# Optimization experiments

Measured on AMD Instinct MI355X. Metric: run time of the kernel, lower is better.

The kernel has to match this reference:

```python
import jax, jax.numpy as jnp
import numpy as np

N_HEADS = 12
MAX_POS = 2048
SEQ = MAX_POS - 2  # seq_len_without_special = 2046
HEAD_DIM = 64
BATCH = 8


def setup_inputs() -> dict:
    key = jax.random.key(0)
    k1, k2, k3 = jax.random.split(key, 3)
    v = jax.random.normal(k1, (BATCH, MAX_POS, N_HEADS, HEAD_DIM), jnp.float32)
    offset = jax.random.normal(k2, (1, N_HEADS), jnp.float32)
    # learned bias base, torch init: uniform(-0.1, 0.1), shape [1, H, SEQ] (symmetric)
    w = jax.random.uniform(k3, (1, N_HEADS, SEQ), jnp.float32, -0.1, 0.1)
    return {"v": v, "offset": offset, "w": w}


def _fft_bias(v, offset, w):
    # strip special tokens ([CLS]/[SEP])
    v_ = v[:, 1:-1, :, :]                      # [B, S, H, D]
    B, S, H, D = v_.shape
    # --- symmetric circulant base z of length 2S-1 ---
    w_ = w[..., :S]                            # [1, H, S]
    z = jnp.concatenate(
        [w_[..., -1:], jnp.flip(w_[..., 1:], axis=-1), w_[..., :-1]], axis=-1
    )                                          # [1, H, 2S-1]
    z = z - offset[..., None]                  # broadcast offset per head
    z = jnp.exp(z)                             # feature_map == 'exp'
    z_fft = jnp.fft.rfft(z)                    # [1, H, S] complex (len 2S-1 odd -> m=S)

    pad = S - 1                                # symmetric: pad_size = seq_len - 1
    v_p = jnp.transpose(v_, (0, 3, 2, 1))      # [B, D, H, S]
    v_p = jnp.pad(v_p, ((0, 0), (0, 0), (0, 0), (pad, 0)))  # left-pad to 2S-1
    v_fft = jnp.fft.rfft(v_p)                  # [B, D, H, S]
    # torch.irfft(x, 1) with default signal_sizes infers even length 2*(m-1)=2S-2
    pbv = jnp.fft.irfft(v_fft * z_fft)[..., :S]  # [B, D, H, S]
    pbv = jnp.pad(pbv, ((0, 0), (0, 0), (0, 0), (1, 1)))     # restore special slots
    pbv = jnp.transpose(pbv, (0, 3, 2, 1))     # [B, S+2, H, D]

    o = jnp.pad(jnp.ones((S,), v.dtype), (pad, 0))           # [2S-1]
    o_fft = jnp.fft.rfft(o)                    # [S]
    z_pb = jnp.fft.irfft(z_fft * o_fft)[..., :S]             # [1, H, S]
    z_pb = jnp.pad(z_pb, ((0, 0), (0, 0), (1, 1)))           # [1, H, S+2]
    z_pb = jnp.swapaxes(z_pb, -2, -1)          # [1, S+2, H]
    return pbv, z_pb


def reference(v, offset, w):
    return _fft_bias(v, offset, w)
```

## Files before the change

kernel.cpp:

```cpp
#include <hip/hip_runtime.h>
#include <hip/hip_bf16.h>

#define BATCH 8
#define MAXPOS 2048
#define SEQ 2046
#define NH 12
#define HD 64
#define CENTER 2047
#define NCSLOT 254
#define TSTEPS 64
#define PLANE (NH * HD)

typedef __attribute__((ext_vector_type(4))) float floatx4;
typedef __attribute__((ext_vector_type(8))) short shortx8;

#define ATILE_BYTES (NH * NCSLOT * 512 * 2)

__global__ __launch_bounds__(256)
void prep_A(const float* __restrict__ w, const float* __restrict__ off,
            ushort* __restrict__ atile) {
    const int cslot = blockIdx.x;
    const int h     = blockIdx.y;
    const int tid   = threadIdx.x;
    const float offh = off[h];
    const float* wh  = w + h * SEQ;
    const int ci   = cslot - 127;
    const int lane = tid >> 2;
    const int jp   = (tid & 3) * 2;
    const int q    = lane >> 4;
    const int m    = lane & 15;
    const int d0   = 16 * ci + q * 8 - m + jp;
    ushort pk[2];
#pragma unroll
    for (int e = 0; e < 2; ++e) {
        int k = d0 + e; k = (k < 0) ? -k : k;
        float val = (k < SEQ) ? __expf(wh[k] - offh) : 0.f;
        __hip_bfloat16 bv = __float2bfloat16(val);
        pk[e] = *(ushort*)&bv;
    }
    *(ushort2*)(atile + ((size_t)(h * NCSLOT + cslot) * 512 + lane * 8 + jp)) = *(ushort2*)pk;
}

__global__ __launch_bounds__(256)
void prep_V(const float* __restrict__ v, ushort* __restrict__ vbf) {
    __shared__ float Ls[32][64];
    const int tc  = blockIdx.x;
    const int h   = blockIdx.y;
    const int b   = blockIdx.z;
    const int tid = threadIdx.x;
#pragma unroll
    for (int i = 0; i < 2; ++i) {
        int idx = tid + 256 * i;
        int row = idx >> 4;
        int c4  = (idx & 15) * 4;
        int t   = tc * 32 + row;
        float4 val = make_float4(0.f, 0.f, 0.f, 0.f);
        if (t < SEQ) val = *(const float4*)(v + ((size_t)(b * MAXPOS + 1 + t) * NH + h) * HD + c4);
        *(float4*)&Ls[row][c4] = val;
    }
    __syncthreads();
    const int wv   = tid >> 6;
    const int lane = tid & 63;
    const int q    = lane >> 4;
    const int dcol = lane & 15;
    ushort pk[8];
#pragma unroll
    for (int j = 0; j < 8; ++j) {
        __hip_bfloat16 bv = __float2bfloat16(Ls[q * 8 + j][wv * 16 + dcol]);
        pk[j] = *(ushort*)&bv;
    }
    *(uint4*)(vbf + ((size_t)((b * NH + h) * TSTEPS + tc) * 4 + wv) * 512 + lane * 8) = *(uint4*)pk;
}

#define LOADA(dst, tc_)                                                        \
    _Pragma("unroll") for (int s = 0; s < 4; ++s)                              \
        dst[s] = *(const shortx8*)(aP + ((tc_) * 2 - s) * 512);
#define LOADB(dst, tc_)                                                        \
    _Pragma("unroll") for (int dt = 0; dt < 4; ++dt)                           \
        dst[dt] = *(const shortx8*)(bP + ((tc_) * 4 + dt) * 512);

__global__ __launch_bounds__(256, 3)
void gemm_pbv(const ushort* __restrict__ atile, const ushort* __restrict__ vbf,
              float* __restrict__ out) {
    const int bid  = blockIdx.x;
    const int slot = bid >> 3;
    const int g    = (bid & 7) * 6 + (slot % 6);
    const int nt   = slot / 6;
    const int h    = g >> 2;
    const int bpair= g & 3;
    const int tid  = threadIdx.x;
    const int wv   = tid >> 6;
    const int lane = tid & 63;
    const int bb   = bpair * 2 + (wv & 1);
    const int sh   = wv >> 1;
    const int sbase= nt * 8 + sh * 4;

    floatx4 acc[4][4];
#pragma unroll
    for (int s = 0; s < 4; ++s)
#pragma unroll
        for (int dt = 0; dt < 4; ++dt) acc[s][dt] = (floatx4){0.f, 0.f, 0.f, 0.f};

    const ushort* aP = atile + ((size_t)h * NCSLOT + (127 - sbase)) * 512 + lane * 8;
    const ushort* bP = vbf + (size_t)(bb * NH + h) * TSTEPS * 4 * 512 + lane * 8;

    shortx8 a0[4], b0[4], a1[4], b1[4];
    LOADA(a0, 0); LOADB(b0, 0);
    for (int tc = 0; tc < TSTEPS; tc += 2) {
        LOADA(a1, tc + 1); LOADB(b1, tc + 1);
#pragma unroll
        for (int s = 0; s < 4; ++s)
#pragma unroll
            for (int dt = 0; dt < 4; ++dt)
                acc[s][dt] = __builtin_amdgcn_mfma_f32_16x16x32_bf16(a0[s], b0[dt], acc[s][dt], 0, 0, 0);
        if (tc + 2 < TSTEPS) { LOADA(a0, tc + 2); LOADB(b0, tc + 2); }
#pragma unroll
        for (int s = 0; s < 4; ++s)
#pragma unroll
            for (int dt = 0; dt < 4; ++dt)
                acc[s][dt] = __builtin_amdgcn_mfma_f32_16x16x32_bf16(a1[s], b1[dt], acc[s][dt], 0, 0, 0);
    }

    const int q    = lane >> 4;
    const int dcol = lane & 15;
    const int n0   = nt * 128 + sh * 64;
#pragma unroll
    for (int s = 0; s < 4; ++s) {
        int nsb = n0 + s * 16 + q * 4;
#pragma unroll
        for (int r = 0; r < 4; ++r) {
            int n = nsb + r;
            if (n < SEQ) {
                float* ob = out + ((size_t)(bb * MAXPOS + 1 + n) * NH + h) * HD + dcol;
#pragma unroll
                for (int dt = 0; dt < 4; ++dt) ob[dt * 16] = acc[s][dt][r];
            }
        }
    }
}

__global__ __launch_bounds__(256)
void zpb_kernel(const float* __restrict__ w, const float* __restrict__ off,
                float* __restrict__ out) {
    __shared__ float Es[SEQ];
    __shared__ float Ss[SEQ];
    __shared__ float wsum[4];
    const int h   = blockIdx.x;
    const int tid = threadIdx.x;
    const int wid = tid >> 6;
    const int lane = tid & 63;
    const float offh = off[h];
    const float* wh  = w + h * SEQ;
    for (int i = tid; i < SEQ; i += 256) Es[i] = __expf(wh[i] - offh);
    __syncthreads();
    const int base = tid * 8;
    float loc[8];
    float s = 0.f;
#pragma unroll
    for (int j = 0; j < 8; ++j) {
        float e = (base + j < SEQ) ? Es[base + j] : 0.f;
        s += e; loc[j] = s;
    }
    float sc = s;
#pragma unroll
    for (int d = 1; d < 64; d <<= 1) {
        float t = __shfl_up(sc, d);
        if (lane >= d) sc += t;
    }
    if (lane == 63) wsum[wid] = sc;
    __syncthreads();
    float woff = 0.f;
    for (int k = 0; k < wid; ++k) woff += wsum[k];
    float prefix = woff + sc - s;
#pragma unroll
    for (int j = 0; j < 8; ++j)
        if (base + j < SEQ) Ss[base + j] = prefix + loc[j];
    __syncthreads();
    const float E0 = Es[0];
    const size_t zb = (size_t)BATCH * MAXPOS * PLANE;
    for (int i = tid; i < SEQ; i += 256)
        out[zb + (size_t)(i + 1) * NH + h] = Ss[i] + Ss[SEQ - 1 - i] - E0;
}

__global__ __launch_bounds__(256)
void zero_bounds_kernel(float* __restrict__ out) {
    const int i = blockIdx.x * 256 + threadIdx.x;
    if (i < 2 * BATCH * PLANE) {
        int side = i / (BATCH * PLANE);
        int r    = i % (BATCH * PLANE);
        int b    = r / PLANE;
        int j    = r % PLANE;
        int p    = side ? (MAXPOS - 1) : 0;
        out[((size_t)b * MAXPOS + p) * PLANE + j] = 0.f;
    }
    if (i < 2 * NH) {
        size_t zb = (size_t)BATCH * MAXPOS * PLANE;
        int p = (i < NH) ? 0 : (MAXPOS - 1);
        out[zb + (size_t)p * NH + (i % NH)] = 0.f;
    }
}

extern "C" void kernel_launch(void* const* d_in, const int* in_sizes, int n_in,
                              void* d_out, int out_size, void* d_ws, size_t ws_size,
                              hipStream_t stream) {
    const float* v   = (const float*)d_in[0];
    const float* off = (const float*)d_in[1];
    const float* w   = (const float*)d_in[2];
    float* out = (float*)d_out;

    ushort* atile = (ushort*)d_ws;
    ushort* vbf   = (ushort*)((char*)d_ws + ATILE_BYTES);

    zero_bounds_kernel<<<48, 256, 0, stream>>>(out);
    zpb_kernel<<<NH, 256, 0, stream>>>(w, off, out);
    prep_A<<<dim3(NCSLOT, NH), 256, 0, stream>>>(w, off, atile);
    prep_V<<<dim3(TSTEPS, NH, BATCH), 256, 0, stream>>>(v, vbf);
    gemm_pbv<<<768, 256, 0, stream>>>(atile, vbf, out);
}
```

Baseline: 155.3 us.

## Fuse small prep kernels and enlarge GEMM per-wave register tile

Merges the zero-bounds, z_pb prefix-sum and A-tile prep kernels into a single launch that dispatches on block index, cutting two kernel launches. The bias GEMM changes from 256-thread blocks with 4x4 tiles per wave to single-wave blocks holding an 8x4 tile for two batches. Each A fragment is now reused across both batches and more rows per load, to reduce global load traffic per MFMA. In exchange, the grid keeps 768 blocks but each is one wave, so the kernel runs far fewer concurrent waves and has much less latency hiding. Accumulator register pressure also rises sharply.

```diff
diff --git a/kernel.cpp b/kernel.cpp
--- a/kernel.cpp
+++ b/kernel.cpp
@@ -6,7 +6,6 @@
 #define SEQ 2046
 #define NH 12
 #define HD 64
-#define CENTER 2047
 #define NCSLOT 254
 #define TSTEPS 64
 #define PLANE (NH * HD)
@@ -17,28 +16,86 @@
 #define ATILE_BYTES (NH * NCSLOT * 512 * 2)
 
 __global__ __launch_bounds__(256)
-void prep_A(const float* __restrict__ w, const float* __restrict__ off,
-            ushort* __restrict__ atile) {
-    const int cslot = blockIdx.x;
-    const int h     = blockIdx.y;
-    const int tid   = threadIdx.x;
-    const float offh = off[h];
-    const float* wh  = w + h * SEQ;
-    const int ci   = cslot - 127;
-    const int lane = tid >> 2;
-    const int jp   = (tid & 3) * 2;
-    const int q    = lane >> 4;
-    const int m    = lane & 15;
-    const int d0   = 16 * ci + q * 8 - m + jp;
-    ushort pk[2];
-#pragma unroll
-    for (int e = 0; e < 2; ++e) {
-        int k = d0 + e; k = (k < 0) ? -k : k;
-        float val = (k < SEQ) ? __expf(wh[k] - offh) : 0.f;
-        __hip_bfloat16 bv = __float2bfloat16(val);
-        pk[e] = *(ushort*)&bv;
-    }
-    *(ushort2*)(atile + ((size_t)(h * NCSLOT + cslot) * 512 + lane * 8 + jp)) = *(ushort2*)pk;
+void small_prep(const float* __restrict__ w, const float* __restrict__ off,
+                ushort* __restrict__ atile, float* __restrict__ out) {
+    __shared__ float Es[SEQ];
+    __shared__ float Ss[SEQ];
+    __shared__ float wsum[4];
+    const int bi  = blockIdx.x;
+    const int tid = threadIdx.x;
+
+    if (bi < NH) {
+        const int h    = bi;
+        const int wid  = tid >> 6;
+        const int lane = tid & 63;
+        const float offh = off[h];
+        const float* wh  = w + h * SEQ;
+        for (int i = tid; i < SEQ; i += 256) Es[i] = __expf(wh[i] - offh);
+        __syncthreads();
+        const int base = tid * 8;
+        float loc[8];
+        float s = 0.f;
+#pragma unroll
+        for (int j = 0; j < 8; ++j) {
+            float e = (base + j < SEQ) ? Es[base + j] : 0.f;
+            s += e; loc[j] = s;
+        }
+        float sc = s;
+#pragma unroll
+        for (int d = 1; d < 64; d <<= 1) {
+            float t = __shfl_up(sc, d);
+            if (lane >= d) sc += t;
+        }
+        if (lane == 63) wsum[wid] = sc;
+        __syncthreads();
+        float woff = 0.f;
+        for (int k = 0; k < wid; ++k) woff += wsum[k];
+        float prefix = woff + sc - s;
+#pragma unroll
+        for (int j = 0; j < 8; ++j)
+            if (base + j < SEQ) Ss[base + j] = prefix + loc[j];
+        __syncthreads();
+        const float E0 = Es[0];
+        const size_t zb = (size_t)BATCH * MAXPOS * PLANE;
+        for (int i = tid; i < SEQ; i += 256)
+            out[zb + (size_t)(i + 1) * NH + h] = Ss[i] + Ss[SEQ - 1 - i] - E0;
+    } else if (bi < NH + NCSLOT * NH) {
+        const int idx   = bi - NH;
+        const int cslot = idx % NCSLOT;
+        const int h     = idx / NCSLOT;
+        const float offh = off[h];
+        const float* wh  = w + h * SEQ;
+        const int ci   = cslot - 127;
+        const int lane = tid >> 2;
+        const int jp   = (tid & 3) * 2;
+        const int q    = lane >> 4;
+        const int m    = lane & 15;
+        const int d0   = 16 * ci + q * 8 - m + jp;
+        ushort pk[2];
+#pragma unroll
+        for (int e = 0; e < 2; ++e) {
+            int k = d0 + e; k = (k < 0) ? -k : k;
+            float val = (k < SEQ) ? __expf(wh[k] - offh) : 0.f;
+            __hip_bfloat16 bv = __float2bfloat16(val);
+            pk[e] = *(ushort*)&bv;
+        }
+        *(ushort2*)(atile + ((size_t)(h * NCSLOT + cslot) * 512 + lane * 8 + jp)) = *(ushort2*)pk;
+    } else {
+        const int i = (bi - NH - NCSLOT * NH) * 256 + tid;
+        if (i < 2 * BATCH * PLANE) {
+            int side = i / (BATCH * PLANE);
+            int r    = i % (BATCH * PLANE);
+            int b    = r / PLANE;
+            int j    = r % PLANE;
+            int p    = side ? (MAXPOS - 1) : 0;
+            out[((size_t)b * MAXPOS + p) * PLANE + j] = 0.f;
+        }
+        if (i < 2 * NH) {
+            size_t zb = (size_t)BATCH * MAXPOS * PLANE;
+            int p = (i < NH) ? 0 : (MAXPOS - 1);
+            out[zb + (size_t)p * NH + (i % NH)] = 0.f;
+        }
+    }
 }
 
 __global__ __launch_bounds__(256)
@@ -72,14 +129,22 @@
     *(uint4*)(vbf + ((size_t)((b * NH + h) * TSTEPS + tc) * 4 + wv) * 512 + lane * 8) = *(uint4*)pk;
 }
 
-#define LOADA(dst, tc_)                                                        \
-    _Pragma("unroll") for (int s = 0; s < 4; ++s)                              \
+#define PREFA(dst, tc_)                                                        \
+    _Pragma("unroll") for (int s = 0; s < 8; ++s)                              \
         dst[s] = *(const shortx8*)(aP + ((tc_) * 2 - s) * 512);
-#define LOADB(dst, tc_)                                                        \
-    _Pragma("unroll") for (int dt = 0; dt < 4; ++dt)                           \
-        dst[dt] = *(const shortx8*)(bP + ((tc_) * 4 + dt) * 512);
-
-__global__ __launch_bounds__(256, 3)
+#define PREFB(dst0, dst1, tc_)                                                 \
+    _Pragma("unroll") for (int dt = 0; dt < 4; ++dt) {                         \
+        dst0[dt] = *(const shortx8*)(bP0 + ((tc_) * 4 + dt) * 512);            \
+        dst1[dt] = *(const shortx8*)(bP1 + ((tc_) * 4 + dt) * 512);            \
+    }
+#define COMPUTE(aa, bb0, bb1)                                                  \
+    _Pragma("unroll") for (int s = 0; s < 8; ++s)                              \
+    _Pragma("unroll") for (int dt = 0; dt < 4; ++dt) {                         \
+        acc[0][s][dt] = __builtin_amdgcn_mfma_f32_16x16x32_bf16(aa[s], bb0[dt], acc[0][s][dt], 0, 0, 0); \
+        acc[1][s][dt] = __builtin_amdgcn_mfma_f32_16x16x32_bf16(aa[s], bb1[dt], acc[1][s][dt], 0, 0, 0); \
+    }
+
+__global__ __launch_bounds__(64, 1)
 void gemm_pbv(const ushort* __restrict__ atile, const ushort* __restrict__ vbf,
               float* __restrict__ out) {
     const int bid  = blockIdx.x;
@@ -87,116 +152,48 @@
     const int g    = (bid & 7) * 6 + (slot % 6);
     const int nt   = slot / 6;
     const int h    = g >> 2;
-    const int bpair= g & 3;
-    const int tid  = threadIdx.x;
-    const int wv   = tid >> 6;
-    const int lane = tid & 63;
-    const int bb   = bpair * 2 + (wv & 1);
-    const int sh   = wv >> 1;
-    const int sbase= nt * 8 + sh * 4;
-
-    floatx4 acc[4][4];
-#pragma unroll
-    for (int s = 0; s < 4; ++s)
-#pragma unroll
-        for (int dt = 0; dt < 4; ++dt) acc[s][dt] = (floatx4){0.f, 0.f, 0.f, 0.f};
-
-    const ushort* aP = atile + ((size_t)h * NCSLOT + (127 - sbase)) * 512 + lane * 8;
-    const ushort* bP = vbf + (size_t)(bb * NH + h) * TSTEPS * 4 * 512 + lane * 8;
-
-    shortx8 a0[4], b0[4], a1[4], b1[4];
-    LOADA(a0, 0); LOADB(b0, 0);
+    const int bp   = g & 3;
+    const int lane = threadIdx.x;
+
+    floatx4 acc[2][8][4];
+#pragma unroll
+    for (int bw = 0; bw < 2; ++bw)
+#pragma unroll
+        for (int s = 0; s < 8; ++s)
+#pragma unroll
+            for (int dt = 0; dt < 4; ++dt) acc[bw][s][dt] = (floatx4){0.f, 0.f, 0.f, 0.f};
+
+    const ushort* aP  = atile + ((size_t)h * NCSLOT + (127 - nt * 8)) * 512 + lane * 8;
+    const ushort* bP0 = vbf + (size_t)(bp * 2 * NH + h) * (TSTEPS * 4 * 512) + lane * 8;
+    const ushort* bP1 = bP0 + (size_t)NH * (TSTEPS * 4 * 512);
+
+    shortx8 a0[8], a1[8], b00[4], b01[4], b10[4], b11[4];
+    PREFA(a0, 0); PREFB(b00, b01, 0);
     for (int tc = 0; tc < TSTEPS; tc += 2) {
-        LOADA(a1, tc + 1); LOADB(b1, tc + 1);
-#pragma unroll
-        for (int s = 0; s < 4; ++s)
-#pragma unroll
-            for (int dt = 0; dt < 4; ++dt)
-                acc[s][dt] = __builtin_amdgcn_mfma_f32_16x16x32_bf16(a0[s], b0[dt], acc[s][dt], 0, 0, 0);
-        if (tc + 2 < TSTEPS) { LOADA(a0, tc + 2); LOADB(b0, tc + 2); }
-#pragma unroll
-        for (int s = 0; s < 4; ++s)
-#pragma unroll
-            for (int dt = 0; dt < 4; ++dt)
-                acc[s][dt] = __builtin_amdgcn_mfma_f32_16x16x32_bf16(a1[s], b1[dt], acc[s][dt], 0, 0, 0);
+        PREFA(a1, tc + 1); PREFB(b10, b11, tc + 1);
+        COMPUTE(a0, b00, b01);
+        if (tc + 2 < TSTEPS) { PREFA(a0, tc + 2); PREFB(b00, b01, tc + 2); }
+        COMPUTE(a1, b10, b11);
     }
 
     const int q    = lane >> 4;
     const int dcol = lane & 15;
-    const int n0   = nt * 128 + sh * 64;
-#pragma unroll
-    for (int s = 0; s < 4; ++s) {
-        int nsb = n0 + s * 16 + q * 4;
-#pragma unroll
-        for (int r = 0; r < 4; ++r) {
-            int n = nsb + r;
-            if (n < SEQ) {
-                float* ob = out + ((size_t)(bb * MAXPOS + 1 + n) * NH + h) * HD + dcol;
-#pragma unroll
-                for (int dt = 0; dt < 4; ++dt) ob[dt * 16] = acc[s][dt][r];
+#pragma unroll
+    for (int bw = 0; bw < 2; ++bw) {
+        const int bb = bp * 2 + bw;
+#pragma unroll
+        for (int s = 0; s < 8; ++s) {
+            int nsb = nt * 128 + s * 16 + q * 4;
+#pragma unroll
+            for (int r = 0; r < 4; ++r) {
+                int n = nsb + r;
+                if (n < SEQ) {
+                    float* ob = out + ((size_t)(bb * MAXPOS + 1 + n) * NH + h) * HD + dcol;
+#pragma unroll
+                    for (int dt = 0; dt < 4; ++dt) ob[dt * 16] = acc[bw][s][dt][r];
+                }
             }
         }
-    }
-}
-
-__global__ __launch_bounds__(256)
-void zpb_kernel(const float* __restrict__ w, const float* __restrict__ off,
-                float* __restrict__ out) {
-    __shared__ float Es[SEQ];
-    __shared__ float Ss[SEQ];
-    __shared__ float wsum[4];
-    const int h   = blockIdx.x;
-    const int tid = threadIdx.x;
-    const int wid = tid >> 6;
-    const int lane = tid & 63;
-    const float offh = off[h];
-    const float* wh  = w + h * SEQ;
-    for (int i = tid; i < SEQ; i += 256) Es[i] = __expf(wh[i] - offh);
-    __syncthreads();
-    const int base = tid * 8;
-    float loc[8];
-    float s = 0.f;
-#pragma unroll
-    for (int j = 0; j < 8; ++j) {
-        float e = (base + j < SEQ) ? Es[base + j] : 0.f;
-        s += e; loc[j] = s;
-    }
-    float sc = s;
-#pragma unroll
-    for (int d = 1; d < 64; d <<= 1) {
-        float t = __shfl_up(sc, d);
-        if (lane >= d) sc += t;
-    }
-    if (lane == 63) wsum[wid] = sc;
-    __syncthreads();
-    float woff = 0.f;
-    for (int k = 0; k < wid; ++k) woff += wsum[k];
-    float prefix = woff + sc - s;
-#pragma unroll
-    for (int j = 0; j < 8; ++j)
-        if (base + j < SEQ) Ss[base + j] = prefix + loc[j];
-    __syncthreads();
-    const float E0 = Es[0];
-    const size_t zb = (size_t)BATCH * MAXPOS * PLANE;
-    for (int i = tid; i < SEQ; i += 256)
-        out[zb + (size_t)(i + 1) * NH + h] = Ss[i] + Ss[SEQ - 1 - i] - E0;
-}
-
-__global__ __launch_bounds__(256)
-void zero_bounds_kernel(float* __restrict__ out) {
-    const int i = blockIdx.x * 256 + threadIdx.x;
-    if (i < 2 * BATCH * PLANE) {
-        int side = i / (BATCH * PLANE);
-        int r    = i % (BATCH * PLANE);
-        int b    = r / PLANE;
-        int j    = r % PLANE;
-        int p    = side ? (MAXPOS - 1) : 0;
-        out[((size_t)b * MAXPOS + p) * PLANE + j] = 0.f;
-    }
-    if (i < 2 * NH) {
-        size_t zb = (size_t)BATCH * MAXPOS * PLANE;
-        int p = (i < NH) ? 0 : (MAXPOS - 1);
-        out[zb + (size_t)p * NH + (i % NH)] = 0.f;
     }
 }
 
@@ -211,9 +208,7 @@
     ushort* atile = (ushort*)d_ws;
     ushort* vbf   = (ushort*)((char*)d_ws + ATILE_BYTES);
 
-    zero_bounds_kernel<<<48, 256, 0, stream>>>(out);
-    zpb_kernel<<<NH, 256, 0, stream>>>(w, off, out);
-    prep_A<<<dim3(NCSLOT, NH), 256, 0, stream>>>(w, off, atile);
+    small_prep<<<NH + NCSLOT * NH + 48, 256, 0, stream>>>(w, off, atile, out);
     prep_V<<<dim3(TSTEPS, NH, BATCH), 256, 0, stream>>>(v, vbf);
-    gemm_pbv<<<768, 256, 0, stream>>>(atile, vbf, out);
-}
+    gemm_pbv<<<768, 64, 0, stream>>>(atile, vbf, out);
+}
```

Result: slower. 175.8 us (+13.2%).

## Merge prep kernels into one launch and stage Toeplitz A tiles through LDS

Applied to the files above, without the earlier changes.

Folds the four small preprocessing kernels (zero bounds, z_pb scan, A-tile build, V transpose to bf16) into one kernel that branches on block index, cutting three launches and their serialization gaps. The GEMM now loads A tiles cooperatively into double-buffered shared memory with global_load_lds, so each wave fetches two tiles instead of four overlapping ones from global. The price is two block barriers per step. The V transpose also gets an XOR swizzle on its LDS staging to reduce bank conflicts. The block-level barriers in the GEMM loop may reduce latency hiding.

```diff
diff --git a/kernel.cpp b/kernel.cpp
--- a/kernel.cpp
+++ b/kernel.cpp
@@ -6,7 +6,6 @@
 #define SEQ 2046
 #define NH 12
 #define HD 64
-#define CENTER 2047
 #define NCSLOT 254
 #define TSTEPS 64
 #define PLANE (NH * HD)
@@ -16,84 +15,145 @@
 
 #define ATILE_BYTES (NH * NCSLOT * 512 * 2)
 
+#define GLOAD_LDS16(src, dst)                                                  \
+    __builtin_amdgcn_global_load_lds(                                          \
+        (const __attribute__((address_space(1))) void*)(src),                  \
+        (__attribute__((address_space(3))) void*)(dst), 16, 0, 0)
+
+#define NB_V   (TSTEPS * NH * BATCH)
+#define NB_ZPB NH
+#define NB_A   (NCSLOT * NH)
+
 __global__ __launch_bounds__(256)
-void prep_A(const float* __restrict__ w, const float* __restrict__ off,
-            ushort* __restrict__ atile) {
-    const int cslot = blockIdx.x;
-    const int h     = blockIdx.y;
-    const int tid   = threadIdx.x;
-    const float offh = off[h];
-    const float* wh  = w + h * SEQ;
-    const int ci   = cslot - 127;
-    const int lane = tid >> 2;
-    const int jp   = (tid & 3) * 2;
-    const int q    = lane >> 4;
-    const int m    = lane & 15;
-    const int d0   = 16 * ci + q * 8 - m + jp;
-    ushort pk[2];
-#pragma unroll
-    for (int e = 0; e < 2; ++e) {
-        int k = d0 + e; k = (k < 0) ? -k : k;
-        float val = (k < SEQ) ? __expf(wh[k] - offh) : 0.f;
-        __hip_bfloat16 bv = __float2bfloat16(val);
-        pk[e] = *(ushort*)&bv;
+void prep_all(const float* __restrict__ v, const float* __restrict__ w,
+              const float* __restrict__ off, ushort* __restrict__ atile,
+              ushort* __restrict__ vbf, float* __restrict__ out) {
+    const int bi  = blockIdx.x;
+    const int tid = threadIdx.x;
+
+    if (bi < NB_V) {
+        __shared__ float Ls[32][64];
+        const int tc = bi & 63;
+        int rem = bi >> 6;
+        const int h = rem % NH;
+        const int b = rem / NH;
+#pragma unroll
+        for (int i = 0; i < 2; ++i) {
+            int idx = tid + 256 * i;
+            int row = idx >> 4;
+            int c4  = (idx & 15) * 4;
+            int key = (row >> 3) * 16;
+            int t   = tc * 32 + row;
+            float4 val = make_float4(0.f, 0.f, 0.f, 0.f);
+            if (t < SEQ) val = *(const float4*)(v + ((size_t)(b * MAXPOS + 1 + t) * NH + h) * HD + c4);
+            *(float4*)&Ls[row][c4 ^ key] = val;
+        }
+        __syncthreads();
+        const int wv   = tid >> 6;
+        const int lane = tid & 63;
+        const int q    = lane >> 4;
+        const int dcol = lane & 15;
+        ushort pk[8];
+#pragma unroll
+        for (int j = 0; j < 8; ++j) {
+            __hip_bfloat16 bv = __float2bfloat16(Ls[q * 8 + j][(wv * 16 + dcol) ^ (q * 16)]);
+            pk[j] = *(ushort*)&bv;
+        }
+        *(uint4*)(vbf + ((size_t)((b * NH + h) * TSTEPS + tc) * 4 + wv) * 512 + lane * 8) = *(uint4*)pk;
+    } else if (bi < NB_V + NB_ZPB) {
+        __shared__ float Es[SEQ];
+        __shared__ float Ss[SEQ];
+        __shared__ float wsum[4];
+        const int h    = bi - NB_V;
+        const int wid  = tid >> 6;
+        const int lane = tid & 63;
+        const float offh = off[h];
+        const float* wh  = w + h * SEQ;
+        for (int i = tid; i < SEQ; i += 256) Es[i] = __expf(wh[i] - offh);
+        __syncthreads();
+        const int base = tid * 8;
+        float loc[8];
+        float s = 0.f;
+#pragma unroll
+        for (int j = 0; j < 8; ++j) {
+            float e = (base + j < SEQ) ? Es[base + j] : 0.f;
+            s += e; loc[j] = s;
+        }
+        float sc = s;
+#pragma unroll
+        for (int d = 1; d < 64; d <<= 1) {
+            float t = __shfl_up(sc, d);
+            if (lane >= d) sc += t;
+        }
+        if (lane == 63) wsum[wid] = sc;
+        __syncthreads();
+        float woff = 0.f;
+        for (int k = 0; k < wid; ++k) woff += wsum[k];
+        float prefix = woff + sc - s;
+#pragma unroll
+        for (int j = 0; j < 8; ++j)
+            if (base + j < SEQ) Ss[base + j] = prefix + loc[j];
+        __syncthreads();
+        const float E0 = Es[0];
+        const size_t zb = (size_t)BATCH * MAXPOS * PLANE;
+        for (int i = tid; i < SEQ; i += 256)
+            out[zb + (size_t)(i + 1) * NH + h] = Ss[i] + Ss[SEQ - 1 - i] - E0;
+    } else if (bi < NB_V + NB_ZPB + NB_A) {
+        const int idx   = bi - NB_V - NB_ZPB;
+        const int cslot = idx % NCSLOT;
+        const int h     = idx / NCSLOT;
+        const float offh = off[h];
+        const float* wh  = w + h * SEQ;
+        const int ci   = cslot - 127;
+        const int lane = tid >> 2;
+        const int jp   = (tid & 3) * 2;
+        const int q    = lane >> 4;
+        const int m    = lane & 15;
+        const int d0   = 16 * ci + q * 8 - m + jp;
+        ushort pk[2];
+#pragma unroll
+        for (int e = 0; e < 2; ++e) {
+            int k = d0 + e; k = (k < 0) ? -k : k;
+            float val = (k < SEQ) ? __expf(wh[k] - offh) : 0.f;
+            __hip_bfloat16 bv = __float2bfloat16(val);
+            pk[e] = *(ushort*)&bv;
+        }
+        *(ushort2*)(atile + ((size_t)(h * NCSLOT + cslot) * 512 + lane * 8 + jp)) = *(ushort2*)pk;
+    } else {
+        const int i = (bi - NB_V - NB_ZPB - NB_A) * 256 + tid;
+        if (i < 2 * BATCH * PLANE) {
+            int side = i / (BATCH * PLANE);
+            int r    = i % (BATCH * PLANE);
+            int b    = r / PLANE;
+            int j    = r % PLANE;
+            int p    = side ? (MAXPOS - 1) : 0;
+            out[((size_t)b * MAXPOS + p) * PLANE + j] = 0.f;
+        }
+        if (i < 2 * NH) {
+            size_t zb = (size_t)BATCH * MAXPOS * PLANE;
+            int p = (i < NH) ? 0 : (MAXPOS - 1);
+            out[zb + (size_t)p * NH + (i % NH)] = 0.f;
+        }
     }
-    *(ushort2*)(atile + ((size_t)(h * NCSLOT + cslot) * 512 + lane * 8 + jp)) = *(ushort2*)pk;
 }
-
-__global__ __launch_bounds__(256)
-void prep_V(const float* __restrict__ v, ushort* __restrict__ vbf) {
-    __shared__ float Ls[32][64];
-    const int tc  = blockIdx.x;
-    const int h   = blockIdx.y;
-    const int b   = blockIdx.z;
-    const int tid = threadIdx.x;
-#pragma unroll
-    for (int i = 0; i < 2; ++i) {
-        int idx = tid + 256 * i;
-        int row = idx >> 4;
-        int c4  = (idx & 15) * 4;
-        int t   = tc * 32 + row;
-        float4 val = make_float4(0.f, 0.f, 0.f, 0.f);
-        if (t < SEQ) val = *(const float4*)(v + ((size_t)(b * MAXPOS + 1 + t) * NH + h) * HD + c4);
-        *(float4*)&Ls[row][c4] = val;
-    }
-    __syncthreads();
-    const int wv   = tid >> 6;
-    const int lane = tid & 63;
-    const int q    = lane >> 4;
-    const int dcol = lane & 15;
-    ushort pk[8];
-#pragma unroll
-    for (int j = 0; j < 8; ++j) {
-        __hip_bfloat16 bv = __float2bfloat16(Ls[q * 8 + j][wv * 16 + dcol]);
-        pk[j] = *(ushort*)&bv;
-    }
-    *(uint4*)(vbf + ((size_t)((b * NH + h) * TSTEPS + tc) * 4 + wv) * 512 + lane * 8) = *(uint4*)pk;
-}
-
-#define LOADA(dst, tc_)                                                        \
-    _Pragma("unroll") for (int s = 0; s < 4; ++s)                              \
-        dst[s] = *(const shortx8*)(aP + ((tc_) * 2 - s) * 512);
-#define LOADB(dst, tc_)                                                        \
-    _Pragma("unroll") for (int dt = 0; dt < 4; ++dt)                           \
-        dst[dt] = *(const shortx8*)(bP + ((tc_) * 4 + dt) * 512);
 
 __global__ __launch_bounds__(256, 3)
 void gemm_pbv(const ushort* __restrict__ atile, const ushort* __restrict__ vbf,
               float* __restrict__ out) {
+    __shared__ short As[2][8 * 512];
+
     const int bid  = blockIdx.x;
     const int slot = bid >> 3;
     const int g    = (bid & 7) * 6 + (slot % 6);
     const int nt   = slot / 6;
     const int h    = g >> 2;
-    const int bpair= g & 3;
+    const int bq   = g & 3;
     const int tid  = threadIdx.x;
     const int wv   = tid >> 6;
     const int lane = tid & 63;
-    const int bb   = bpair * 2 + (wv & 1);
     const int sh   = wv >> 1;
-    const int sbase= nt * 8 + sh * 4;
+    const int bw   = wv & 1;
+    const int bb   = bq * 2 + bw;
 
     floatx4 acc[4][4];
 #pragma unroll
@@ -101,32 +161,59 @@
 #pragma unroll
         for (int dt = 0; dt < 4; ++dt) acc[s][dt] = (floatx4){0.f, 0.f, 0.f, 0.f};
 
-    const ushort* aP = atile + ((size_t)h * NCSLOT + (127 - sbase)) * 512 + lane * 8;
-    const ushort* bP = vbf + (size_t)(bb * NH + h) * TSTEPS * 4 * 512 + lane * 8;
-
-    shortx8 a0[4], b0[4], a1[4], b1[4];
-    LOADA(a0, 0); LOADB(b0, 0);
+    const ushort* aS = atile + ((size_t)h * NCSLOT + (127 - nt * 8 - 2 * wv)) * 512 + lane * 8;
+    const ushort* bP = vbf + (size_t)(bb * NH + h) * (TSTEPS * 4 * 512) + lane * 8;
+    short* aW0 = &As[0][2 * wv * 512];
+    short* aW1 = &As[1][2 * wv * 512];
+    const short* aR0 = &As[0][sh * 4 * 512] + lane * 8;
+    const short* aR1 = &As[1][sh * 4 * 512] + lane * 8;
+
+    shortx8 a[4], b0[4], b1[4];
+
+    GLOAD_LDS16(aS, aW0);
+    GLOAD_LDS16(aS - 512, aW0 + 512);
+#pragma unroll
+    for (int dt = 0; dt < 4; ++dt) b0[dt] = *(const shortx8*)(bP + dt * 512);
+    __syncthreads();
+
     for (int tc = 0; tc < TSTEPS; tc += 2) {
-        LOADA(a1, tc + 1); LOADB(b1, tc + 1);
+        GLOAD_LDS16(aS + (tc + 1) * 1024, aW1);
+        GLOAD_LDS16(aS + (tc + 1) * 1024 - 512, aW1 + 512);
+#pragma unroll
+        for (int dt = 0; dt < 4; ++dt)
+            b1[dt] = *(const shortx8*)(bP + (tc + 1) * 2048 + dt * 512);
+#pragma unroll
+        for (int s = 0; s < 4; ++s) a[s] = *(const shortx8*)(aR0 + s * 512);
 #pragma unroll
         for (int s = 0; s < 4; ++s)
 #pragma unroll
             for (int dt = 0; dt < 4; ++dt)
-                acc[s][dt] = __builtin_amdgcn_mfma_f32_16x16x32_bf16(a0[s], b0[dt], acc[s][dt], 0, 0, 0);
-        if (tc + 2 < TSTEPS) { LOADA(a0, tc + 2); LOADB(b0, tc + 2); }
+                acc[s][dt] = __builtin_amdgcn_mfma_f32_16x16x32_bf16(a[s], b0[dt], acc[s][dt], 0, 0, 0);
+        __syncthreads();
+
+        if (tc + 2 < TSTEPS) {
+            GLOAD_LDS16(aS + (tc + 2) * 1024, aW0);
+            GLOAD_LDS16(aS + (tc + 2) * 1024 - 512, aW0 + 512);
+#pragma unroll
+            for (int dt = 0; dt < 4; ++dt)
+                b0[dt] = *(const shortx8*)(bP + (tc + 2) * 2048 + dt * 512);
+        }
+#pragma unroll
+        for (int s = 0; s < 4; ++s) a[s] = *(const shortx8*)(aR1 + s * 512);
 #pragma unroll
         for (int s = 0; s < 4; ++s)
 #pragma unroll
             for (int dt = 0; dt < 4; ++dt)
-                acc[s][dt] = __builtin_amdgcn_mfma_f32_16x16x32_bf16(a1[s], b1[dt], acc[s][dt], 0, 0, 0);
+                acc[s][dt] = __builtin_amdgcn_mfma_f32_16x16x32_bf16(a[s], b1[dt], acc[s][dt], 0, 0, 0);
+        __syncthreads();
     }
 
     const int q    = lane >> 4;
     const int dcol = lane & 15;
-    const int n0   = nt * 128 + sh * 64;
+    const int nB   = nt * 128 + sh * 64;
 #pragma unroll
     for (int s = 0; s < 4; ++s) {
-        int nsb = n0 + s * 16 + q * 4;
+        int nsb = nB + s * 16 + q * 4;
 #pragma unroll
         for (int r = 0; r < 4; ++r) {
             int n = nsb + r;
@@ -136,67 +223,6 @@
                 for (int dt = 0; dt < 4; ++dt) ob[dt * 16] = acc[s][dt][r];
             }
         }
-    }
-}
-
-__global__ __launch_bounds__(256)
-void zpb_kernel(const float* __restrict__ w, const float* __restrict__ off,
-                float* __restrict__ out) {
-    __shared__ float Es[SEQ];
-    __shared__ float Ss[SEQ];
-    __shared__ float wsum[4];
-    const int h   = blockIdx.x;
-    const int tid = threadIdx.x;
-    const int wid = tid >> 6;
-    const int lane = tid & 63;
-    const float offh = off[h];
-    const float* wh  = w + h * SEQ;
-    for (int i = tid; i < SEQ; i += 256) Es[i] = __expf(wh[i] - offh);
-    __syncthreads();
-    const int base = tid * 8;
-    float loc[8];
-    float s = 0.f;
-#pragma unroll
-    for (int j = 0; j < 8; ++j) {
-        float e = (base + j < SEQ) ? Es[base + j] : 0.f;
-        s += e; loc[j] = s;
-    }
-    float sc = s;
-#pragma unroll
-    for (int d = 1; d < 64; d <<= 1) {
-        float t = __shfl_up(sc, d);
-        if (lane >= d) sc += t;
-    }
-    if (lane == 63) wsum[wid] = sc;
-    __syncthreads();
-    float woff = 0.f;
-    for (int k = 0; k < wid; ++k) woff += wsum[k];
-    float prefix = woff + sc - s;
-#pragma unroll
-    for (int j = 0; j < 8; ++j)
-        if (base + j < SEQ) Ss[base + j] = prefix + loc[j];
-    __syncthreads();
-    const float E0 = Es[0];
-    const size_t zb = (size_t)BATCH * MAXPOS * PLANE;
-    for (int i = tid; i < SEQ; i += 256)
-        out[zb + (size_t)(i + 1) * NH + h] = Ss[i] + Ss[SEQ - 1 - i] - E0;
-}
-
-__global__ __launch_bounds__(256)
-void zero_bounds_kernel(float* __restrict__ out) {
-    const int i = blockIdx.x * 256 + threadIdx.x;
-    if (i < 2 * BATCH * PLANE) {
-        int side = i / (BATCH * PLANE);
-        int r    = i % (BATCH * PLANE);
-        int b    = r / PLANE;
-        int j    = r % PLANE;
-        int p    = side ? (MAXPOS - 1) : 0;
-        out[((size_t)b * MAXPOS + p) * PLANE + j] = 0.f;
-    }
-    if (i < 2 * NH) {
-        size_t zb = (size_t)BATCH * MAXPOS * PLANE;
-        int p = (i < NH) ? 0 : (MAXPOS - 1);
-        out[zb + (size_t)p * NH + (i % NH)] = 0.f;
     }
 }
 
@@ -211,9 +237,6 @@
     ushort* atile = (ushort*)d_ws;
     ushort* vbf   = (ushort*)((char*)d_ws + ATILE_BYTES);
 
-    zero_bounds_kernel<<<48, 256, 0, stream>>>(out);
-    zpb_kernel<<<NH, 256, 0, stream>>>(w, off, out);
-    prep_A<<<dim3(NCSLOT, NH), 256, 0, stream>>>(w, off, atile);
-    prep_V<<<dim3(TSTEPS, NH, BATCH), 256, 0, stream>>>(v, vbf);
+    prep_all<<<NB_V + NB_ZPB + NB_A + 48, 256, 0, stream>>>(v, w, off, atile, vbf, out);
     gemm_pbv<<<768, 256, 0, stream>>>(atile, vbf, out);
 }
```

Measured after the change: 145.8 us. 1.07x faster.
